# Performance work log

Measured on AMD Instinct MI355X. Metric: run time of the kernel, lower is better.

## Reference

```python
import jax, jax.numpy as jnp
import numpy as np

N_NODES = 40000
N_EDGES = 640000
D_MODEL = 128
N_LAYERS = 2


def setup_inputs() -> dict:
    key = jax.random.key(0)
    k1, k2, k3 = jax.random.split(key, 3)
    x = jax.random.normal(k1, (N_NODES, D_MODEL), dtype=jnp.float32)
    # Glorot-ish scaled weights per layer
    W = jax.random.normal(k2, (N_LAYERS, D_MODEL, D_MODEL), dtype=jnp.float32) / np.sqrt(D_MODEL)
    b = jnp.zeros((N_LAYERS, D_MODEL), dtype=jnp.float32)
    edge_index = jax.random.randint(k3, (2, N_EDGES), 0, N_NODES, dtype=jnp.int64)
    return {"x": x, "W": W, "b": b, "edge_index": edge_index}


def reference(x, W, b, edge_index):
    """Stacked DGL-style GraphConv (norm='both') layers on a flattened batched graph.

    Per layer: h' = D_in^{-1/2} A D_out^{-1/2} (h W) + b
    implemented as gather(src) -> per-edge normalize -> segment_sum(dst).
    """
    src = edge_index[0]
    dst = edge_index[1]
    n = x.shape[0]
    ones = jnp.ones((src.shape[0],), dtype=x.dtype)
    deg_out = jax.ops.segment_sum(ones, src, num_segments=n)  # out-degree of src nodes
    deg_in = jax.ops.segment_sum(ones, dst, num_segments=n)   # in-degree of dst nodes
    # symmetric normalization per edge: 1/sqrt(d_out(u) * d_in(v)), clipped to avoid div0
    edge_norm = jax.lax.rsqrt(jnp.clip(deg_out[src] * deg_in[dst], 1.0, None))  # [E]

    h = x
    for l in range(W.shape[0]):
        m = h @ W[l]                                   # [N, d] dense transform
        msg = m[src] * edge_norm[:, None]              # [E, d] gather + scale
        h = jax.ops.segment_sum(msg, dst, num_segments=n) + b[l]  # [N, d] scatter-add
    return h
```

## Files before the change

kernel.cpp:

```cpp
#include <hip/hip_runtime.h>
#include <hip/hip_fp16.h>

#define D_MODEL 128
#define NREP 8
#define FC 32
#define WCB 8

__device__ __forceinline__ bool sniff_i64(const void* ei) {
    const long long* p64 = (const long long*)ei;
    bool f64 = true;
#pragma unroll
    for (int i = 0; i < 8; ++i) {
        long long v = p64[i];
        f64 = f64 && (v >= 0 && v < (1LL << 31));
    }
    return f64;
}

__device__ __forceinline__ void load_edge(const void* ei, int e, int nE, bool f64,
                                          int& s, int& d) {
    if (f64) {
        const long long* p64 = (const long long*)ei;
        s = (int)p64[e];
        d = (int)p64[(size_t)nE + e];
    } else {
        const int* p32 = (const int*)ei;
        s = p32[e];
        d = p32[(size_t)nE + e];
    }
}

__global__ __launch_bounds__(1024) void hist_wc_kernel(const void* __restrict__ ei,
                                                       unsigned int* __restrict__ Cpk,
                                                       const float* __restrict__ W,
                                                       const float* __restrict__ b,
                                                       float* __restrict__ wc,
                                                       int nE, int n) {
    if (blockIdx.x >= FC) {
        int gid = (blockIdx.x - FC) * 1024 + threadIdx.x;
        const float* W2 = W + 128 * 128;
        for (int g = gid; g < 129 * 128; g += WCB * 1024) {
            int r = g >> 7, j = g & 127;
            const float* lhs = (r < 128) ? (W + (size_t)r * 128) : b;
            float acc = 0.f;
#pragma unroll 4
            for (int k = 0; k < 128; ++k) acc = fmaf(lhs[k], W2[(size_t)k * 128 + j], acc);
            wc[g] = acc;
        }
        return;
    }
    extern __shared__ unsigned int h[];
    bool f64 = sniff_i64(ei);
    int chunk = blockIdx.x;
    for (int i = threadIdx.x; i < n; i += 1024) h[i] = 0;
    __syncthreads();
    int ech = (nE + FC - 1) / FC;
    int e0 = chunk * ech;
    int e1 = min(nE, e0 + ech);
    if (f64) {
        const long long* p64 = (const long long*)ei;
        for (int e = e0 + threadIdx.x; e < e1; e += 1024) {
            atomicAdd(&h[(int)p64[e]], 1u);
            atomicAdd(&h[(int)p64[(size_t)nE + e]], 0x10000u);
        }
    } else {
        const int* p32 = (const int*)ei;
        for (int e = e0 + threadIdx.x; e < e1; e += 1024) {
            atomicAdd(&h[p32[e]], 1u);
            atomicAdd(&h[p32[(size_t)nE + e]], 0x10000u);
        }
    }
    __syncthreads();
    unsigned int* C = Cpk + (size_t)chunk * n;
    for (int i = threadIdx.x; i < n; i += 1024) C[i] = h[i];
}

__global__ __launch_bounds__(1024) void scanA_xcvt_kernel(const unsigned int* __restrict__ Cpk,
                                                          const float* __restrict__ x,
                                                          float* __restrict__ a,
                                                          float* __restrict__ bfac,
                                                          float* __restrict__ ab,
                                                          int* __restrict__ deg_in,
                                                          int* __restrict__ part,
                                                          float2* __restrict__ xh, int n) {
    __shared__ int wsum[16];
    __shared__ float sh_a[1024];
    int tid = threadIdx.x;
    int i = blockIdx.x * 1024 + tid;
    int lane = tid & 63, wid = tid >> 6;
    int din = 0;
    float fa = 0.f;
    if (i < n) {
        int dout = 0;
#pragma unroll 8
        for (int c = 0; c < FC; ++c) {
            unsigned int w = Cpk[(size_t)c * n + i];
            dout += (int)(w & 0xFFFFu);
            din += (int)(w >> 16);
        }
        fa = rsqrtf((float)max(dout, 1));
        float fb = rsqrtf((float)max(din, 1));
        a[i] = fa;
        bfac[i] = fb;
        ab[i] = fa * fb;
        deg_in[i] = din;
    }
    sh_a[tid] = fa;
    int v = din;
#pragma unroll
    for (int d = 32; d > 0; d >>= 1) v += __shfl_down(v, d, 64);
    if (lane == 0) wsum[wid] = v;
    __syncthreads();
    if (tid == 0) {
        int s = 0;
#pragma unroll
        for (int w = 0; w < 16; ++w) s += wsum[w];
        part[blockIdx.x] = s;
    }
    int rows_in_block = min(1024, n - blockIdx.x * 1024);
    if (rows_in_block <= 0) return;
    int total = rows_in_block * 32;
    const float4* xb = (const float4*)(x + (size_t)blockIdx.x * 1024 * D_MODEL);
    float2* xhb = xh + (size_t)blockIdx.x * 1024 * 32;
    for (int t = tid; t < total; t += 1024) {
        int rl = t >> 5;
        float s = sh_a[rl];
        float4 vv = xb[t];
        union { __half2 h2[2]; float2 f2; } u;
        u.h2[0] = __floats2half2_rn(s * vv.x, s * vv.y);
        u.h2[1] = __floats2half2_rn(s * vv.z, s * vv.w);
        xhb[t] = u.f2;
    }
}

__global__ __launch_bounds__(1024) void scanBC_kernel(const int* __restrict__ deg,
                                                      const int* __restrict__ part,
                                                      const unsigned int* __restrict__ Cpk,
                                                      int* __restrict__ offs,
                                                      int* __restrict__ base, int n) {
    __shared__ int wsum[16];
    __shared__ int blk_prefix;
    int tid = threadIdx.x;
    int i = blockIdx.x * 1024 + tid;
    int lane = tid & 63, wid = tid >> 6;
    if (tid == 0) {
        int acc = 0;
        for (int j = 0; j < (int)blockIdx.x; ++j) acc += part[j];
        blk_prefix = acc;
    }
    int v = (i < n) ? deg[i] : 0;
    int s = v;
#pragma unroll
    for (int d = 1; d < 64; d <<= 1) {
        int t = __shfl_up(s, d, 64);
        if (lane >= d) s += t;
    }
    if (lane == 63) wsum[wid] = s;
    __syncthreads();
    if (wid == 0) {
        int wsv = (lane < 16) ? wsum[lane] : 0;
#pragma unroll
        for (int d = 1; d < 16; d <<= 1) {
            int t = __shfl_up(wsv, d, 16);
            if ((lane & 15) >= d) wsv += t;
        }
        if (lane < 16) wsum[lane] = wsv;
    }
    __syncthreads();
    int pfx = blk_prefix + ((wid > 0) ? wsum[wid - 1] : 0);
    int incl = pfx + s;
    if (i < n) {
        int run = incl - v;
        offs[i] = run;
        if (i == n - 1) offs[n] = incl;
#pragma unroll 8
        for (int c = 0; c < FC; ++c) {
            base[(size_t)c * n + i] = run;
            run += (int)(Cpk[(size_t)c * n + i] >> 16);
        }
    }
}

__global__ __launch_bounds__(1024) void fill_lds_kernel(const void* __restrict__ ei,
                                                        const int* __restrict__ base,
                                                        int* __restrict__ csr_src,
                                                        int nE, int n) {
    extern __shared__ int cur[];
    bool f64 = sniff_i64(ei);
    int chunk = blockIdx.x;
    for (int i = threadIdx.x; i < n; i += 1024) cur[i] = base[(size_t)chunk * n + i];
    __syncthreads();
    int ech = (nE + FC - 1) / FC;
    int e0 = chunk * ech;
    int e1 = min(nE, e0 + ech);
    for (int e = e0 + threadIdx.x; e < e1; e += 1024) {
        int s, d;
        load_edge(ei, e, nE, f64, s, d);
        int slot = atomicAdd(&cur[d], 1);
        csr_src[slot] = s;
    }
}

template <int MODE>
__global__ __launch_bounds__(256) void agg_kernel(const __half2* __restrict__ rows_in,
                                                  const int* __restrict__ offs,
                                                  const int* __restrict__ csr,
                                                  const float* __restrict__ ab,
                                                  const float* __restrict__ bfac,
                                                  const float* __restrict__ a_arr,
                                                  __half2* __restrict__ out_rows,
                                                  float* __restrict__ c_out, int n) {
    int node = blockIdx.x * 4 + (threadIdx.x >> 6);
    if (node >= n) return;
    node = __builtin_amdgcn_readfirstlane(node);
    int lane = threadIdx.x & 63;
    const __half2* rl = rows_in + lane;
    int beg = offs[node], end = offs[node + 1];
    float ax0 = 0.f, ay0 = 0.f, ax1 = 0.f, ay1 = 0.f;
    float ax2 = 0.f, ay2 = 0.f, ax3 = 0.f, ay3 = 0.f;
    float cs = 0.f;
    int e = beg;
    for (; e + 7 < end; e += 8) {
        int s0 = csr[e],     s1 = csr[e + 1], s2 = csr[e + 2], s3 = csr[e + 3];
        int s4 = csr[e + 4], s5 = csr[e + 5], s6 = csr[e + 6], s7 = csr[e + 7];
        __half2 v0 = rl[(size_t)s0 * 64];
        __half2 v1 = rl[(size_t)s1 * 64];
        __half2 v2 = rl[(size_t)s2 * 64];
        __half2 v3 = rl[(size_t)s3 * 64];
        __half2 v4 = rl[(size_t)s4 * 64];
        __half2 v5 = rl[(size_t)s5 * 64];
        __half2 v6 = rl[(size_t)s6 * 64];
        __half2 v7 = rl[(size_t)s7 * 64];
        float2 f0 = __half22float2(v0), f1 = __half22float2(v1);
        float2 f2 = __half22float2(v2), f3 = __half22float2(v3);
        float2 f4 = __half22float2(v4), f5 = __half22float2(v5);
        float2 f6 = __half22float2(v6), f7 = __half22float2(v7);
        ax0 += f0.x + f4.x; ay0 += f0.y + f4.y;
        ax1 += f1.x + f5.x; ay1 += f1.y + f5.y;
        ax2 += f2.x + f6.x; ay2 += f2.y + f6.y;
        ax3 += f3.x + f7.x; ay3 += f3.y + f7.y;
        if (MODE == 1)
            cs += ((a_arr[s0] + a_arr[s1]) + (a_arr[s2] + a_arr[s3])) +
                  ((a_arr[s4] + a_arr[s5]) + (a_arr[s6] + a_arr[s7]));
    }
    for (; e + 1 < end; e += 2) {
        int s0 = csr[e], s1 = csr[e + 1];
        float2 f0 = __half22float2(rl[(size_t)s0 * 64]);
        float2 f1 = __half22float2(rl[(size_t)s1 * 64]);
        ax0 += f0.x; ay0 += f0.y;
        ax1 += f1.x; ay1 += f1.y;
        if (MODE == 1) cs += a_arr[s0] + a_arr[s1];
    }
    if (e < end) {
        int s0 = csr[e];
        float2 f0 = __half22float2(rl[(size_t)s0 * 64]);
        ax0 += f0.x; ay0 += f0.y;
        if (MODE == 1) cs += a_arr[s0];
    }
    float sx = (ax0 + ax1) + (ax2 + ax3);
    float sy = (ay0 + ay1) + (ay2 + ay3);
    if (MODE == 0) {
        float sc = ab[node];
        out_rows[(size_t)node * 64 + lane] = __floats2half2_rn(sc * sx, sc * sy);
    } else {
        out_rows[(size_t)node * 64 + lane] = __floats2half2_rn(sx, sy);
        if (lane == 0) c_out[node] = bfac[node] * cs;
    }
}

__global__ __launch_bounds__(256) void gemm_final_kernel(const __half2* __restrict__ A2,
                                                         const float* __restrict__ wc,
                                                         const float* __restrict__ bfac,
                                                         const float* __restrict__ c_arr,
                                                         const float* __restrict__ b2,
                                                         float* __restrict__ out, int nRows) {
    __shared__ float Ws[32][128];
    __shared__ float At[32][36];
    int tid = threadIdx.x;
    int tc = tid & 31;
    int tr = tid >> 5;
    int row0 = blockIdx.x * 32;
    float acc[4][4] = {};

    for (int k0 = 0; k0 < D_MODEL; k0 += 32) {
        __syncthreads();
        {
            const float4* Wg = (const float4*)(wc + (size_t)k0 * D_MODEL);
            float4* WsV = (float4*)&Ws[0][0];
#pragma unroll
            for (int i = 0; i < 4; ++i) WsV[tid + 256 * i] = Wg[tid + 256 * i];
        }
        int k0h = k0 >> 1;
#pragma unroll
        for (int i = 0; i < 2; ++i) {
            int lin = tid + 256 * i;
            int r = lin >> 4;
            int h = lin & 15;
            int row = row0 + r;
            __half2 v = (row < nRows) ? A2[(size_t)row * 64 + k0h + h]
                                      : __floats2half2_rn(0.f, 0.f);
            float2 f = __half22float2(v);
            At[2 * h][r] = f.x;
            At[2 * h + 1][r] = f.y;
        }
        __syncthreads();
#pragma unroll
        for (int kk = 0; kk < 32; ++kk) {
            float4 w4 = *(const float4*)&Ws[kk][4 * tc];
            float4 a4 = *(const float4*)&At[kk][4 * tr];
            float wv[4] = {w4.x, w4.y, w4.z, w4.w};
            float av[4] = {a4.x, a4.y, a4.z, a4.w};
#pragma unroll
            for (int i = 0; i < 4; ++i)
#pragma unroll
                for (int j = 0; j < 4; ++j)
                    acc[i][j] = fmaf(av[i], wv[j], acc[i][j]);
        }
    }
    float4 g4 = *(const float4*)(wc + 128 * 128 + 4 * tc);
    float4 b4 = *(const float4*)(b2 + 4 * tc);
#pragma unroll
    for (int i = 0; i < 4; ++i) {
        int row = row0 + 4 * tr + i;
        if (row < nRows) {
            float bf = bfac[row];
            float cv = c_arr[row];
            float4 o;
            o.x = bf * acc[i][0] + cv * g4.x + b4.x;
            o.y = bf * acc[i][1] + cv * g4.y + b4.y;
            o.z = bf * acc[i][2] + cv * g4.z + b4.z;
            o.w = bf * acc[i][3] + cv * g4.w + b4.w;
            *(float4*)(out + (size_t)row * D_MODEL + 4 * tc) = o;
        }
    }
}

__global__ void prep_kernel(const void* __restrict__ ei, int* __restrict__ rep_out,
                            int* __restrict__ rep_in, int nE, int n) {
    bool f64 = sniff_i64(ei);
    int e = blockIdx.x * blockDim.x + threadIdx.x;
    if (e >= nE) return;
    int s, d;
    load_edge(ei, e, nE, f64, s, d);
    int rep = blockIdx.x & (NREP - 1);
    atomicAdd(&rep_out[(size_t)rep * n + s], 1);
    atomicAdd(&rep_in[(size_t)rep * n + d], 1);
}

__global__ void deg_reduce_rep_kernel(const int* __restrict__ rep_out,
                                      const int* __restrict__ rep_in,
                                      float* __restrict__ a, float* __restrict__ bfac,
                                      float* __restrict__ ab, int* __restrict__ deg_in,
                                      int n) {
    int v = blockIdx.x * blockDim.x + threadIdx.x;
    if (v >= n) return;
    int dout = 0, din = 0;
#pragma unroll
    for (int r = 0; r < NREP; ++r) {
        dout += rep_out[(size_t)r * n + v];
        din += rep_in[(size_t)r * n + v];
    }
    float fa = rsqrtf((float)max(dout, 1));
    float fb = rsqrtf((float)max(din, 1));
    a[v] = fa;
    bfac[v] = fb;
    ab[v] = fa * fb;
    deg_in[v] = din;
}

__global__ __launch_bounds__(1024) void scanA_plain_kernel(const int* __restrict__ deg,
                                                           int* __restrict__ part, int n) {
    __shared__ int wsum[16];
    int i = blockIdx.x * 1024 + threadIdx.x;
    int lane = threadIdx.x & 63, wid = threadIdx.x >> 6;
    int v = (i < n) ? deg[i] : 0;
#pragma unroll
    for (int d = 32; d > 0; d >>= 1) v += __shfl_down(v, d, 64);
    if (lane == 0) wsum[wid] = v;
    __syncthreads();
    if (threadIdx.x == 0) {
        int s = 0;
#pragma unroll
        for (int w = 0; w < 16; ++w) s += wsum[w];
        part[blockIdx.x] = s;
    }
}

__global__ __launch_bounds__(1024) void scanC_plain_kernel(const int* __restrict__ deg,
                                                           const int* __restrict__ part,
                                                           int* __restrict__ offs, int n) {
    __shared__ int wsum[16];
    __shared__ int blk_prefix;
    int i = blockIdx.x * 1024 + threadIdx.x;
    int lane = threadIdx.x & 63, wid = threadIdx.x >> 6;
    if (threadIdx.x == 0) {
        int acc = 0;
        for (int j = 0; j < (int)blockIdx.x; ++j) acc += part[j];
        blk_prefix = acc;
    }
    int v = (i < n) ? deg[i] : 0;
    int s = v;
#pragma unroll
    for (int d = 1; d < 64; d <<= 1) {
        int t = __shfl_up(s, d, 64);
        if (lane >= d) s += t;
    }
    if (lane == 63) wsum[wid] = s;
    __syncthreads();
    if (wid == 0) {
        int wsv = (lane < 16) ? wsum[lane] : 0;
#pragma unroll
        for (int d = 1; d < 16; d <<= 1) {
            int t = __shfl_up(wsv, d, 16);
            if ((lane & 15) >= d) wsv += t;
        }
        if (lane < 16) wsum[lane] = wsv;
    }
    __syncthreads();
    int pfx = blk_prefix + ((wid > 0) ? wsum[wid - 1] : 0);
    int incl = pfx + s;
    if (i < n) {
        offs[i] = incl - v;
        if (i == n - 1) offs[n] = incl;
    }
}

__global__ void fill_kernel(const void* __restrict__ ei, const int* __restrict__ offs,
                            int* __restrict__ cursor, int* __restrict__ csr_src, int nE) {
    bool f64 = sniff_i64(ei);
    int e = blockIdx.x * blockDim.x + threadIdx.x;
    if (e >= nE) return;
    int s, d;
    load_edge(ei, e, nE, f64, s, d);
    int slot = offs[d] + atomicAdd(&cursor[d], 1);
    csr_src[slot] = s;
}

__global__ void xcvt_kernel(const float* __restrict__ x, const float* __restrict__ a,
                            float2* __restrict__ xh, int n4) {
    int idx = blockIdx.x * blockDim.x + threadIdx.x;
    if (idx >= n4) return;
    int row = idx >> 5;
    float s = a[row];
    float4 v = ((const float4*)x)[idx];
    union { __half2 h2[2]; float2 f2; } uu;
    uu.h2[0] = __floats2half2_rn(s * v.x, s * v.y);
    uu.h2[1] = __floats2half2_rn(s * v.z, s * v.w);
    xh[idx] = uu.f2;
}

__global__ void wc_plain_kernel(const float* __restrict__ W, const float* __restrict__ b,
                                float* __restrict__ wc) {
    int gid = blockIdx.x * blockDim.x + threadIdx.x;
    if (gid >= 129 * 128) return;
    int r = gid >> 7, j = gid & 127;
    const float* W2 = W + 128 * 128;
    const float* lhs = (r < 128) ? (W + (size_t)r * 128) : b;
    float acc = 0.f;
#pragma unroll 4
    for (int k = 0; k < 128; ++k) acc = fmaf(lhs[k], W2[(size_t)k * 128 + j], acc);
    wc[gid] = acc;
}

extern "C" void kernel_launch(void* const* d_in, const int* in_sizes, int n_in,
                              void* d_out, int out_size, void* d_ws, size_t ws_size,
                              hipStream_t stream) {
    const float* x = (const float*)d_in[0];
    const float* W = (const float*)d_in[1];
    const float* b = (const float*)d_in[2];
    const void* ei = d_in[3];
    const int D = D_MODEL;
    int N = in_sizes[0] / D;
    int E = in_sizes[3] / 2;
    float* out = (float*)d_out;

    char* p = (char*)d_ws;
    size_t off = 0;
    auto take = [&](size_t bytes) {
        void* r = p + off;
        off += (bytes + 255) & ~(size_t)255;
        return r;
    };
    __half2* xh   = (__half2*)take((size_t)N * D * 2);
    __half2* u    = (__half2*)take((size_t)N * D * 2);
    int* csr_src  = (int*)take((size_t)E * 4);
    float* a_arr  = (float*)take((size_t)N * 4);
    float* bfac   = (float*)take((size_t)N * 4);
    float* ab     = (float*)take((size_t)N * 4);
    float* c_arr  = (float*)take((size_t)N * 4);
    int* deg_in   = (int*)take((size_t)N * 4);
    int* offs     = (int*)take((size_t)(N + 1) * 4);
    int* cursor   = (int*)take((size_t)N * 4);
    int* part     = (int*)take(256 * 4);
    float* wc     = (float*)take((size_t)129 * 128 * 4);
    unsigned int* Cpk = (unsigned int*)take((size_t)FC * N * 4);
    int* base     = (int*)take((size_t)FC * N * 4);
    size_t lds_need = off;
    __half2* t2 = xh;

    size_t lds_bytes = (size_t)N * 4;
    bool use_lds = (lds_bytes <= 160000) && (lds_need <= ws_size);

    int eb = (E + 255) / 256;
    int G = (N + 1023) / 1024;

    if (use_lds) {
        hist_wc_kernel<<<FC + WCB, 1024, lds_bytes, stream>>>(ei, Cpk, W, b, wc, E, N);
        scanA_xcvt_kernel<<<G, 1024, 0, stream>>>(Cpk, x, a_arr, bfac, ab, deg_in,
                                                  part, (float2*)xh, N);
        scanBC_kernel<<<G, 1024, 0, stream>>>(deg_in, part, Cpk, offs, base, N);
        fill_lds_kernel<<<FC, 1024, lds_bytes, stream>>>(ei, base, csr_src, E, N);
    } else {
        int* rep_out = (int*)Cpk;
        int* rep_in  = (int*)base;
        if (lds_need > ws_size) {
            rep_out = (int*)u;
            rep_in  = (int*)((char*)u + (size_t)NREP * N * 4);
        }
        hipMemsetAsync(rep_out, 0, (size_t)NREP * N * 4, stream);
        hipMemsetAsync(rep_in, 0, (size_t)NREP * N * 4, stream);
        hipMemsetAsync(cursor, 0, (size_t)N * 4, stream);
        wc_plain_kernel<<<(129 * 128 + 255) / 256, 256, 0, stream>>>(W, b, wc);
        prep_kernel<<<eb, 256, 0, stream>>>(ei, rep_out, rep_in, E, N);
        deg_reduce_rep_kernel<<<(N + 255) / 256, 256, 0, stream>>>(rep_out, rep_in, a_arr,
                                                                   bfac, ab, deg_in, N);
        scanA_plain_kernel<<<G, 1024, 0, stream>>>(deg_in, part, N);
        scanC_plain_kernel<<<G, 1024, 0, stream>>>(deg_in, part, offs, N);
        fill_kernel<<<eb, 256, 0, stream>>>(ei, offs, cursor, csr_src, E);
        int n4 = N * (D / 4);
        xcvt_kernel<<<(n4 + 255) / 256, 256, 0, stream>>>(x, a_arr, (float2*)xh, n4);
    }

    agg_kernel<0><<<(N + 3) / 4, 256, 0, stream>>>(xh, offs, csr_src, ab, bfac, a_arr,
                                                   u, c_arr, N);
    agg_kernel<1><<<(N + 3) / 4, 256, 0, stream>>>(u, offs, csr_src, ab, bfac, a_arr,
                                                   t2, c_arr, N);
    gemm_final_kernel<<<(N + 31) / 32, 256, 0, stream>>>(t2, wc, bfac, c_arr,
                                                         b + 128, out, N);
}
```

Baseline: 149.1 us.

## Split aggregation into feature quarters with edge-parallel lanes per wavefront

The aggregation kernel now launches four times as many blocks. Each block handles one 32-column quarter of the feature row, and the four 16-lane groups in a wavefront process different edges in parallel before a shuffle reduction. The goal is to run the grid in feature-quarter order, so each pass touches a quarter of the source rows and is more likely to hit in cache, with more edges in flight per wave. The cost is re-reading the CSR indices and offsets four times, narrower 64-byte row segments per gather, and only 16 lanes doing the stores.

```diff
diff --git a/kernel.cpp b/kernel.cpp
--- a/kernel.cpp
+++ b/kernel.cpp
@@ -202,69 +202,58 @@
 }
 
 template <int MODE>
-__global__ __launch_bounds__(256) void agg_kernel(const __half2* __restrict__ rows_in,
-                                                  const int* __restrict__ offs,
-                                                  const int* __restrict__ csr,
-                                                  const float* __restrict__ ab,
-                                                  const float* __restrict__ bfac,
-                                                  const float* __restrict__ a_arr,
-                                                  __half2* __restrict__ out_rows,
-                                                  float* __restrict__ c_out, int n) {
-    int node = blockIdx.x * 4 + (threadIdx.x >> 6);
+__global__ __launch_bounds__(256) void aggq_kernel(const __half2* __restrict__ rows_in,
+                                                   const int* __restrict__ offs,
+                                                   const int* __restrict__ csr,
+                                                   const float* __restrict__ ab,
+                                                   const float* __restrict__ bfac,
+                                                   const float* __restrict__ a_arr,
+                                                   __half2* __restrict__ out_rows,
+                                                   float* __restrict__ c_out,
+                                                   int n, int nbq) {
+    int bid = blockIdx.x;
+    int q = bid / nbq;
+    int nb = bid - q * nbq;
+    int node = nb * 4 + (threadIdx.x >> 6);
     if (node >= n) return;
     node = __builtin_amdgcn_readfirstlane(node);
     int lane = threadIdx.x & 63;
-    const __half2* rl = rows_in + lane;
+    int g = lane >> 4;
+    int f = lane & 15;
     int beg = offs[node], end = offs[node + 1];
-    float ax0 = 0.f, ay0 = 0.f, ax1 = 0.f, ay1 = 0.f;
-    float ax2 = 0.f, ay2 = 0.f, ax3 = 0.f, ay3 = 0.f;
-    float cs = 0.f;
-    int e = beg;
-    for (; e + 7 < end; e += 8) {
-        int s0 = csr[e],     s1 = csr[e + 1], s2 = csr[e + 2], s3 = csr[e + 3];
-        int s4 = csr[e + 4], s5 = csr[e + 5], s6 = csr[e + 6], s7 = csr[e + 7];
-        __half2 v0 = rl[(size_t)s0 * 64];
-        __half2 v1 = rl[(size_t)s1 * 64];
-        __half2 v2 = rl[(size_t)s2 * 64];
-        __half2 v3 = rl[(size_t)s3 * 64];
-        __half2 v4 = rl[(size_t)s4 * 64];
-        __half2 v5 = rl[(size_t)s5 * 64];
-        __half2 v6 = rl[(size_t)s6 * 64];
-        __half2 v7 = rl[(size_t)s7 * 64];
-        float2 f0 = __half22float2(v0), f1 = __half22float2(v1);
-        float2 f2 = __half22float2(v2), f3 = __half22float2(v3);
-        float2 f4 = __half22float2(v4), f5 = __half22float2(v5);
-        float2 f6 = __half22float2(v6), f7 = __half22float2(v7);
-        ax0 += f0.x + f4.x; ay0 += f0.y + f4.y;
-        ax1 += f1.x + f5.x; ay1 += f1.y + f5.y;
-        ax2 += f2.x + f6.x; ay2 += f2.y + f6.y;
-        ax3 += f3.x + f7.x; ay3 += f3.y + f7.y;
-        if (MODE == 1)
-            cs += ((a_arr[s0] + a_arr[s1]) + (a_arr[s2] + a_arr[s3])) +
-                  ((a_arr[s4] + a_arr[s5]) + (a_arr[s6] + a_arr[s7]));
-    }
-    for (; e + 1 < end; e += 2) {
-        int s0 = csr[e], s1 = csr[e + 1];
-        float2 f0 = __half22float2(rl[(size_t)s0 * 64]);
-        float2 f1 = __half22float2(rl[(size_t)s1 * 64]);
-        ax0 += f0.x; ay0 += f0.y;
-        ax1 += f1.x; ay1 += f1.y;
-        if (MODE == 1) cs += a_arr[s0] + a_arr[s1];
+    const __half2* tb = rows_in + q * 16 + f;
+    float ax = 0.f, ay = 0.f, cs = 0.f;
+    int e = beg + g;
+    for (; e + 4 < end; e += 8) {
+        int s0 = csr[e];
+        int s1 = csr[e + 4];
+        float2 f0 = __half22float2(tb[(size_t)s0 * 64]);
+        float2 f1 = __half22float2(tb[(size_t)s1 * 64]);
+        ax += f0.x + f1.x;
+        ay += f0.y + f1.y;
+        if (MODE == 1 && f == 0) cs += a_arr[s0] + a_arr[s1];
     }
     if (e < end) {
         int s0 = csr[e];
-        float2 f0 = __half22float2(rl[(size_t)s0 * 64]);
-        ax0 += f0.x; ay0 += f0.y;
-        if (MODE == 1) cs += a_arr[s0];
-    }
-    float sx = (ax0 + ax1) + (ax2 + ax3);
-    float sy = (ay0 + ay1) + (ay2 + ay3);
+        float2 f0 = __half22float2(tb[(size_t)s0 * 64]);
+        ax += f0.x;
+        ay += f0.y;
+        if (MODE == 1 && f == 0) cs += a_arr[s0];
+    }
+    ax += __shfl_xor(ax, 32); ax += __shfl_xor(ax, 16);
+    ay += __shfl_xor(ay, 32); ay += __shfl_xor(ay, 16);
     if (MODE == 0) {
-        float sc = ab[node];
-        out_rows[(size_t)node * 64 + lane] = __floats2half2_rn(sc * sx, sc * sy);
+        if (lane < 16) {
+            float sc = ab[node];
+            out_rows[(size_t)node * 64 + q * 16 + lane] = __floats2half2_rn(sc * ax, sc * ay);
+        }
     } else {
-        out_rows[(size_t)node * 64 + lane] = __floats2half2_rn(sx, sy);
-        if (lane == 0) c_out[node] = bfac[node] * cs;
+        if (lane < 16)
+            out_rows[(size_t)node * 64 + q * 16 + lane] = __floats2half2_rn(ax, ay);
+        if (q == 0) {
+            cs += __shfl_xor(cs, 32); cs += __shfl_xor(cs, 16);
+            if (lane == 0) c_out[node] = bfac[node] * cs;
+        }
     }
 }
 
@@ -531,10 +520,11 @@
         xcvt_kernel<<<(n4 + 255) / 256, 256, 0, stream>>>(x, a_arr, (float2*)xh, n4);
     }
 
-    agg_kernel<0><<<(N + 3) / 4, 256, 0, stream>>>(xh, offs, csr_src, ab, bfac, a_arr,
-                                                   u, c_arr, N);
-    agg_kernel<1><<<(N + 3) / 4, 256, 0, stream>>>(u, offs, csr_src, ab, bfac, a_arr,
-                                                   t2, c_arr, N);
+    int nbq = (N + 3) / 4;
+    aggq_kernel<0><<<4 * nbq, 256, 0, stream>>>(xh, offs, csr_src, ab, bfac, a_arr,
+                                                u, c_arr, N, nbq);
+    aggq_kernel<1><<<4 * nbq, 256, 0, stream>>>(u, offs, csr_src, ab, bfac, a_arr,
+                                                t2, c_arr, N, nbq);
     gemm_final_kernel<<<(N + 31) / 32, 256, 0, stream>>>(t2, wc, bfac, c_arr,
                                                          b + 128, out, N);
 }
```

New measurement: 226.6 us. +52.0%, slower.
